# Optimization experiments

Measured on AMD Instinct MI355X. Metric: run time of the kernel, lower is better.

## Reference

```python
import jax, jax.numpy as jnp
import numpy as np

N_NODES = 100000
N_EDGES = 300000


def _nnconv(x, src, dst, edge_attr, w, b, root, bias, in_dim, out_dim):
    # PyG NNConv with aggr='add': W_e = nn(edge_attr_e).reshape(in, out)
    # msg_e = x[src_e] @ W_e ; out_i = sum_e->i msg_e + x_i @ root + bias
    W = (edge_attr @ w.T + b).reshape(-1, in_dim, out_dim)        # [E, in, out]
    msg = jnp.einsum('ei,eio->eo', x[src], W)                     # [E, out]
    agg = jax.ops.segment_sum(msg, dst, num_segments=x.shape[0])  # [N, out]
    return agg + x @ root + bias


def setup_inputs() -> dict:
    key = jax.random.key(0)
    ks = jax.random.split(key, 16)
    x = jax.random.normal(ks[0], (N_NODES, 2), dtype=jnp.float32)
    edge_index = jax.random.randint(ks[1], (2, N_EDGES), 0, N_NODES)
    edge_attr = jax.random.uniform(ks[2], (N_EDGES, 2), dtype=jnp.float32)

    def lin(k, out_d, in_d):
        s = 1.0 / np.sqrt(in_d)
        kw, kb = jax.random.split(k)
        w = jax.random.uniform(kw, (out_d, in_d), minval=-s, maxval=s)
        b = jax.random.uniform(kb, (out_d,), minval=-s, maxval=s)
        return w, b

    nn1_w, nn1_b = lin(ks[3], 64, 2)      # edge MLP for conv1: 2 -> 2*32
    nn2_w, nn2_b = lin(ks[4], 1024, 2)    # edge MLP for conv2: 2 -> 32*32
    root1 = jax.random.normal(ks[5], (2, 32)) * (1.0 / np.sqrt(2))
    bias1 = jnp.zeros((32,), dtype=jnp.float32)
    root2 = jax.random.normal(ks[6], (32, 32)) * (1.0 / np.sqrt(32))
    bias2 = jnp.zeros((32,), dtype=jnp.float32)
    fc1_w, fc1_b = lin(ks[7], 32, 32)
    fc2_w, fc2_b = lin(ks[8], 1, 32)
    return {
        'x': x, 'edge_index': edge_index, 'edge_attr': edge_attr,
        'nn1_w': nn1_w, 'nn1_b': nn1_b, 'root1': root1, 'bias1': bias1,
        'nn2_w': nn2_w, 'nn2_b': nn2_b, 'root2': root2, 'bias2': bias2,
        'fc1_w': fc1_w, 'fc1_b': fc1_b, 'fc2_w': fc2_w, 'fc2_b': fc2_b,
    }


def reference(x, edge_index, edge_attr, nn1_w, nn1_b, root1, bias1,
              nn2_w, nn2_b, root2, bias2, fc1_w, fc1_b, fc2_w, fc2_b):
    src, dst = edge_index[0], edge_index[1]
    h = jax.nn.relu(_nnconv(x, src, dst, edge_attr, nn1_w, nn1_b, root1, bias1, 2, 32))
    h = jax.nn.relu(_nnconv(h, src, dst, edge_attr, nn2_w, nn2_b, root2, bias2, 32, 32))
    h = jax.nn.relu(h @ fc1_w.T + fc1_b)
    return h @ fc2_w.T + fc2_b  # [N, 1]
```

## Files before the change

### kernel.cpp

```cpp
#include <hip/hip_runtime.h>

#define N_NODES 100000
#define N_EDGES 300000
#define CAP 32
#define NPAIRS (N_NODES / 2)
#define NT 64
#define NTILES ((N_NODES + NT - 1) / NT)
#define PAD 129

__global__ __launch_bounds__(256) void zero_cnt_kernel(int4* __restrict__ p,
                                                       int n4)
{
    int i = blockIdx.x * 256 + threadIdx.x;
    if (i < n4) p[i] = make_int4(0, 0, 0, 0);
}

__global__ __launch_bounds__(256) void scatter_kernel(
    const int* __restrict__ src, const int* __restrict__ dst,
    const float* __restrict__ ea,
    int* __restrict__ cnt, float4* __restrict__ slots)
{
    int e = blockIdx.x * 256 + threadIdx.x;
    if (e >= N_EDGES) return;
    int s = src[e], d = dst[e];
    float2 a = ((const float2*)ea)[e];
    int pos = atomicAdd(&cnt[d], 1);
    if (pos < CAP)
        slots[(size_t)d * CAP + pos] = make_float4(__int_as_float(s), a.x, a.y, 0.f);
}

__global__ __launch_bounds__(256) void prepack_kernel(
    const float* __restrict__ nn2_w, const float* __restrict__ nn2_b,
    const float* __restrict__ root2, const float* __restrict__ fc1_w,
    float* __restrict__ Wt, float* __restrict__ Ft)
{
    int t = blockIdx.x * 256 + threadIdx.x;
    if (t < 4096) {
        int i = t >> 5, o = t & 31;
        int ii = i & 31;
        float v;
        if (i < 32)      v = nn2_w[(ii * 32 + o) * 2];
        else if (i < 64) v = nn2_w[(ii * 32 + o) * 2 + 1];
        else if (i < 96) v = nn2_b[ii * 32 + o];
        else             v = root2[ii * 32 + o];
        Wt[i * 32 + o] = v;
    }
    if (t < 1024) {
        int o = t >> 5, j = t & 31;
        Ft[o * 32 + j] = fc1_w[j * 32 + o];
    }
}

__global__ __launch_bounds__(256) void layer1a_kernel(
    const float* __restrict__ x, const int* __restrict__ cnt,
    const float4* __restrict__ slots,
    const float* __restrict__ nn1_w, const float* __restrict__ nn1_b,
    const float* __restrict__ root1, const float* __restrict__ bias1,
    float* __restrict__ h1)
{
    int t = threadIdx.x;
    int wv = t >> 6, lane = t & 63, o = lane & 31, hihalf = lane >> 5;
    int pair = blockIdx.x * 4 + wv;
    if (pair >= NPAIRS) return;
    int n = pair * 2 + hihalf;
    int c = min(cnt[n], CAP);
    float u0 = 0.f, u1 = 0.f, u2 = 0.f, u3 = 0.f, u4 = 0.f, u5 = 0.f;
    if (o < c) {
        float4 sl = slots[(size_t)n * CAP + o];
        int s = __float_as_int(sl.x);
        float2 xv = ((const float2*)x)[s];
        u0 = xv.x * sl.y; u1 = xv.x * sl.z;
        u2 = xv.y * sl.y; u3 = xv.y * sl.z;
        u4 = xv.x;        u5 = xv.y;
    }
    #pragma unroll
    for (int m = 1; m < 32; m <<= 1) {
        u0 += __shfl_xor(u0, m, 32);
        u1 += __shfl_xor(u1, m, 32);
        u2 += __shfl_xor(u2, m, 32);
        u3 += __shfl_xor(u3, m, 32);
        u4 += __shfl_xor(u4, m, 32);
        u5 += __shfl_xor(u5, m, 32);
    }
    float2 w0 = ((const float2*)nn1_w)[o];
    float2 w1 = ((const float2*)nn1_w)[32 + o];
    float2 xn = ((const float2*)x)[n];
    float agg = u0 * w0.x + u1 * w0.y + u2 * w1.x + u3 * w1.y
              + u4 * nn1_b[o] + u5 * nn1_b[32 + o];
    float h = agg + fmaf(xn.x, root1[o], fmaf(xn.y, root1[32 + o], bias1[o]));
    h1[(size_t)n * 32 + o] = fmaxf(h, 0.f);
}

__global__ __launch_bounds__(512) void fused2_kernel(
    const float* __restrict__ h1, const int* __restrict__ cnt,
    const float4* __restrict__ slots,
    const float* __restrict__ Wt, const float* __restrict__ Ft,
    const float* __restrict__ bias2,
    const float* __restrict__ fc1_b, const float* __restrict__ fc2_w,
    const float* __restrict__ fc2_b, float* __restrict__ out)
{
    __shared__ float ld[NT][PAD];
    __shared__ float h2s[NT][33];
    float* psf = &ld[0][0];

    int t = threadIdx.x;
    int hw = t >> 5;
    int o  = t & 31;
    int wv = t >> 6;
    int wvu = __builtin_amdgcn_readfirstlane(wv);
    int lane = t & 63;
    int tb = blockIdx.x * NT;

    int na = tb + hw, nb = tb + 16 + hw, nc = tb + 32 + hw, nd = tb + 48 + hw;
    int ca = (na < N_NODES) ? cnt[na] : 0;
    int cb2 = (nb < N_NODES) ? cnt[nb] : 0;
    int cc = (nc < N_NODES) ? cnt[nc] : 0;
    int cd = (nd < N_NODES) ? cnt[nd] : 0;
    #pragma unroll
    for (int r = 0; r < 4; ++r) {
        int ln = r * 16 + hw;
        int n = tb + ln;
        int c = (r == 0) ? ca : (r == 1) ? cb2 : (r == 2) ? cc : cd;
        c = min(c, CAP);
        if (n < N_NODES) {
            float U = 0.f, V = 0.f, Wc = 0.f;
            for (int j0 = 0; j0 < c; j0 += 4) {
                bool g1 = j0 + 1 < c, g2 = j0 + 2 < c, g3 = j0 + 3 < c;
                float4 s0 = slots[(size_t)n * CAP + j0];
                float4 s1 = g1 ? slots[(size_t)n * CAP + j0 + 1] : s0;
                float4 s2 = g2 ? slots[(size_t)n * CAP + j0 + 2] : s0;
                float4 s3 = g3 ? slots[(size_t)n * CAP + j0 + 3] : s0;
                int i0 = __float_as_int(s0.x), i1 = __float_as_int(s1.x);
                int i2 = __float_as_int(s2.x), i3 = __float_as_int(s3.x);
                float v0 = h1[(size_t)i0 * 32 + o];
                float v1 = h1[(size_t)i1 * 32 + o];
                float v2 = h1[(size_t)i2 * 32 + o];
                float v3 = h1[(size_t)i3 * 32 + o];
                U = fmaf(s0.y, v0, U);
                U = fmaf(g1 ? s1.y : 0.f, v1, U);
                U = fmaf(g2 ? s2.y : 0.f, v2, U);
                U = fmaf(g3 ? s3.y : 0.f, v3, U);
                V = fmaf(s0.z, v0, V);
                V = fmaf(g1 ? s1.z : 0.f, v1, V);
                V = fmaf(g2 ? s2.z : 0.f, v2, V);
                V = fmaf(g3 ? s3.z : 0.f, v3, V);
                Wc += v0;
                Wc = fmaf(g1 ? 1.f : 0.f, v1, Wc);
                Wc = fmaf(g2 ? 1.f : 0.f, v2, Wc);
                Wc = fmaf(g3 ? 1.f : 0.f, v3, Wc);
            }
            float T = h1[(size_t)n * 32 + o];
            ld[ln][o]      = U;
            ld[ln][32 + o] = V;
            ld[ln][64 + o] = Wc;
            ld[ln][96 + o] = T;
        }
    }
    __syncthreads();

    {
        int cb = 4 * wvu;
        float4 bb = *(const float4*)(bias2 + cb);
        float a0 = bb.x, a1 = bb.y, a2 = bb.z, a3 = bb.w;
        for (int i = 0; i < 128; ++i) {
            float hv = ld[lane][i];
            float4 wA = *(const float4*)(Wt + i * 32 + cb);
            a0 = fmaf(hv, wA.x, a0); a1 = fmaf(hv, wA.y, a1);
            a2 = fmaf(hv, wA.z, a2); a3 = fmaf(hv, wA.w, a3);
        }
        h2s[lane][cb + 0] = fmaxf(a0, 0.f);
        h2s[lane][cb + 1] = fmaxf(a1, 0.f);
        h2s[lane][cb + 2] = fmaxf(a2, 0.f);
        h2s[lane][cb + 3] = fmaxf(a3, 0.f);
    }
    __syncthreads();

    {
        int cb = 4 * wvu;
        float4 fb = *(const float4*)(fc1_b + cb);
        float z0 = fb.x, z1 = fb.y, z2 = fb.z, z3 = fb.w;
        for (int i = 0; i < 32; ++i) {
            float hv = h2s[lane][i];
            float4 fA = *(const float4*)(Ft + i * 32 + cb);
            z0 = fmaf(hv, fA.x, z0); z1 = fmaf(hv, fA.y, z1);
            z2 = fmaf(hv, fA.z, z2); z3 = fmaf(hv, fA.w, z3);
        }
        float4 cw = *(const float4*)(fc2_w + cb);
        float po = fmaxf(z0, 0.f) * cw.x + fmaxf(z1, 0.f) * cw.y
                 + fmaxf(z2, 0.f) * cw.z + fmaxf(z3, 0.f) * cw.w;
        psf[wv * NT + lane] = po;
    }
    __syncthreads();
    if (wv == 0) {
        int n = tb + lane;
        if (n < N_NODES) {
            float s = psf[lane]            + psf[NT + lane]
                    + psf[2 * NT + lane]   + psf[3 * NT + lane]
                    + psf[4 * NT + lane]   + psf[5 * NT + lane]
                    + psf[6 * NT + lane]   + psf[7 * NT + lane];
            out[n] = s + fc2_b[0];
        }
    }
}

extern "C" void kernel_launch(void* const* d_in, const int* in_sizes, int n_in,
                              void* d_out, int out_size, void* d_ws, size_t ws_size,
                              hipStream_t stream) {
    const float* x      = (const float*)d_in[0];
    const int*   ei     = (const int*)d_in[1];
    const float* ea     = (const float*)d_in[2];
    const float* nn1_w  = (const float*)d_in[3];
    const float* nn1_b  = (const float*)d_in[4];
    const float* root1  = (const float*)d_in[5];
    const float* bias1  = (const float*)d_in[6];
    const float* nn2_w  = (const float*)d_in[7];
    const float* nn2_b  = (const float*)d_in[8];
    const float* root2  = (const float*)d_in[9];
    const float* bias2  = (const float*)d_in[10];
    const float* fc1_w  = (const float*)d_in[11];
    const float* fc1_b  = (const float*)d_in[12];
    const float* fc2_w  = (const float*)d_in[13];
    const float* fc2_b  = (const float*)d_in[14];
    float* out = (float*)d_out;

    float* ws = (float*)d_ws;
    int*    cnt   = (int*)ws;
    float4* slots = (float4*)(ws + 262144);
    float*  h1    = ws + 262144 + (size_t)N_NODES * CAP * 4;
    float*  Wt    = h1 + (size_t)N_NODES * 32;
    float*  Ft    = Wt + 4096;

    const int* src = ei;
    const int* dst = ei + N_EDGES;

    zero_cnt_kernel<<<(N_NODES / 4 + 255) / 256, 256, 0, stream>>>(
        (int4*)cnt, N_NODES / 4);
    prepack_kernel<<<16, 256, 0, stream>>>(
        nn2_w, nn2_b, root2, fc1_w, Wt, Ft);
    scatter_kernel<<<(N_EDGES + 255) / 256, 256, 0, stream>>>(
        src, dst, ea, cnt, slots);
    layer1a_kernel<<<(NPAIRS + 3) / 4, 256, 0, stream>>>(
        x, cnt, slots, nn1_w, nn1_b, root1, bias1, h1);
    fused2_kernel<<<NTILES, 512, 0, stream>>>(
        h1, cnt, slots, Wt, Ft, bias2, fc1_b, fc2_w, fc2_b, out);
}
```

Measured before the change: 96.06 us.

## Split fused layer-2 kernel into separate gather and matvec/FC kernels

Splits the fused second-layer kernel into a gather kernel that writes per-node U/V/W aggregates to a global buffer and a dense matvec/FC kernel that loads them coalesced into shared memory. The intent is to give the irregular gather higher occupancy, free of the large LDS footprint and block-wide syncs, and to make the dense stage regular. The cost is an extra global round trip of about 96 floats per node and an extra launch. Inner loops are also unrolled, and the last tile reads past the valid nodes into adjacent workspace.

```diff
diff --git a/kernel.cpp b/kernel.cpp
--- a/kernel.cpp
+++ b/kernel.cpp
@@ -91,9 +91,48 @@
     h1[(size_t)n * 32 + o] = fmaxf(h, 0.f);
 }
 
-__global__ __launch_bounds__(512) void fused2_kernel(
+__global__ __launch_bounds__(256) void gather_uvw_kernel(
     const float* __restrict__ h1, const int* __restrict__ cnt,
-    const float4* __restrict__ slots,
+    const float4* __restrict__ slots, float* __restrict__ UVW)
+{
+    int t = threadIdx.x, o = t & 31;
+    int n = blockIdx.x * 8 + (t >> 5);
+    if (n >= N_NODES) return;
+    int c = min(cnt[n], CAP);
+    float U = 0.f, V = 0.f, W = 0.f;
+    for (int j0 = 0; j0 < c; j0 += 4) {
+        bool g1 = j0 + 1 < c, g2 = j0 + 2 < c, g3 = j0 + 3 < c;
+        float4 s0 = slots[(size_t)n * CAP + j0];
+        float4 s1 = g1 ? slots[(size_t)n * CAP + j0 + 1] : s0;
+        float4 s2 = g2 ? slots[(size_t)n * CAP + j0 + 2] : s0;
+        float4 s3 = g3 ? slots[(size_t)n * CAP + j0 + 3] : s0;
+        int i0 = __float_as_int(s0.x), i1 = __float_as_int(s1.x);
+        int i2 = __float_as_int(s2.x), i3 = __float_as_int(s3.x);
+        float v0 = h1[(size_t)i0 * 32 + o];
+        float v1 = h1[(size_t)i1 * 32 + o];
+        float v2 = h1[(size_t)i2 * 32 + o];
+        float v3 = h1[(size_t)i3 * 32 + o];
+        U = fmaf(s0.y, v0, U);
+        U = fmaf(g1 ? s1.y : 0.f, v1, U);
+        U = fmaf(g2 ? s2.y : 0.f, v2, U);
+        U = fmaf(g3 ? s3.y : 0.f, v3, U);
+        V = fmaf(s0.z, v0, V);
+        V = fmaf(g1 ? s1.z : 0.f, v1, V);
+        V = fmaf(g2 ? s2.z : 0.f, v2, V);
+        V = fmaf(g3 ? s3.z : 0.f, v3, V);
+        W += v0;
+        W = fmaf(g1 ? 1.f : 0.f, v1, W);
+        W = fmaf(g2 ? 1.f : 0.f, v2, W);
+        W = fmaf(g3 ? 1.f : 0.f, v3, W);
+    }
+    size_t b = (size_t)n * 96;
+    UVW[b + o]      = U;
+    UVW[b + 32 + o] = V;
+    UVW[b + 64 + o] = W;
+}
+
+__global__ __launch_bounds__(512, 6) void matvec_fc_kernel(
+    const float* __restrict__ UVW, const float* __restrict__ h1,
     const float* __restrict__ Wt, const float* __restrict__ Ft,
     const float* __restrict__ bias2,
     const float* __restrict__ fc1_b, const float* __restrict__ fc2_w,
@@ -104,57 +143,30 @@
     float* psf = &ld[0][0];
 
     int t = threadIdx.x;
-    int hw = t >> 5;
-    int o  = t & 31;
     int wv = t >> 6;
     int wvu = __builtin_amdgcn_readfirstlane(wv);
     int lane = t & 63;
     int tb = blockIdx.x * NT;
 
-    int na = tb + hw, nb = tb + 16 + hw, nc = tb + 32 + hw, nd = tb + 48 + hw;
-    int ca = (na < N_NODES) ? cnt[na] : 0;
-    int cb2 = (nb < N_NODES) ? cnt[nb] : 0;
-    int cc = (nc < N_NODES) ? cnt[nc] : 0;
-    int cd = (nd < N_NODES) ? cnt[nd] : 0;
-    #pragma unroll
-    for (int r = 0; r < 4; ++r) {
-        int ln = r * 16 + hw;
-        int n = tb + ln;
-        int c = (r == 0) ? ca : (r == 1) ? cb2 : (r == 2) ? cc : cd;
-        c = min(c, CAP);
-        if (n < N_NODES) {
-            float U = 0.f, V = 0.f, Wc = 0.f;
-            for (int j0 = 0; j0 < c; j0 += 4) {
-                bool g1 = j0 + 1 < c, g2 = j0 + 2 < c, g3 = j0 + 3 < c;
-                float4 s0 = slots[(size_t)n * CAP + j0];
-                float4 s1 = g1 ? slots[(size_t)n * CAP + j0 + 1] : s0;
-                float4 s2 = g2 ? slots[(size_t)n * CAP + j0 + 2] : s0;
-                float4 s3 = g3 ? slots[(size_t)n * CAP + j0 + 3] : s0;
-                int i0 = __float_as_int(s0.x), i1 = __float_as_int(s1.x);
-                int i2 = __float_as_int(s2.x), i3 = __float_as_int(s3.x);
-                float v0 = h1[(size_t)i0 * 32 + o];
-                float v1 = h1[(size_t)i1 * 32 + o];
-                float v2 = h1[(size_t)i2 * 32 + o];
-                float v3 = h1[(size_t)i3 * 32 + o];
-                U = fmaf(s0.y, v0, U);
-                U = fmaf(g1 ? s1.y : 0.f, v1, U);
-                U = fmaf(g2 ? s2.y : 0.f, v2, U);
-                U = fmaf(g3 ? s3.y : 0.f, v3, U);
-                V = fmaf(s0.z, v0, V);
-                V = fmaf(g1 ? s1.z : 0.f, v1, V);
-                V = fmaf(g2 ? s2.z : 0.f, v2, V);
-                V = fmaf(g3 ? s3.z : 0.f, v3, V);
-                Wc += v0;
-                Wc = fmaf(g1 ? 1.f : 0.f, v1, Wc);
-                Wc = fmaf(g2 ? 1.f : 0.f, v2, Wc);
-                Wc = fmaf(g3 ? 1.f : 0.f, v3, Wc);
-            }
-            float T = h1[(size_t)n * 32 + o];
-            ld[ln][o]      = U;
-            ld[ln][32 + o] = V;
-            ld[ln][64 + o] = Wc;
-            ld[ln][96 + o] = T;
-        }
+    {
+        const float4* uvw4 = (const float4*)(UVW + (size_t)tb * 96);
+        #pragma unroll
+        for (int it = 0; it < 3; ++it) {
+            int f4i = it * 512 + t;
+            float4 v = uvw4[f4i];
+            int node = f4i / 24, c4 = (f4i % 24) * 4;
+            ld[node][c4]     = v.x;
+            ld[node][c4 + 1] = v.y;
+            ld[node][c4 + 2] = v.z;
+            ld[node][c4 + 3] = v.w;
+        }
+        const float4* h14 = (const float4*)(h1 + (size_t)tb * 32);
+        float4 v = h14[t];
+        int node = t >> 3, c4 = 96 + (t & 7) * 4;
+        ld[node][c4]     = v.x;
+        ld[node][c4 + 1] = v.y;
+        ld[node][c4 + 2] = v.z;
+        ld[node][c4 + 3] = v.w;
     }
     __syncthreads();
 
@@ -162,6 +174,7 @@
         int cb = 4 * wvu;
         float4 bb = *(const float4*)(bias2 + cb);
         float a0 = bb.x, a1 = bb.y, a2 = bb.z, a3 = bb.w;
+        #pragma unroll 8
         for (int i = 0; i < 128; ++i) {
             float hv = ld[lane][i];
             float4 wA = *(const float4*)(Wt + i * 32 + cb);
@@ -179,6 +192,7 @@
         int cb = 4 * wvu;
         float4 fb = *(const float4*)(fc1_b + cb);
         float z0 = fb.x, z1 = fb.y, z2 = fb.z, z3 = fb.w;
+        #pragma unroll 8
         for (int i = 0; i < 32; ++i) {
             float hv = h2s[lane][i];
             float4 fA = *(const float4*)(Ft + i * 32 + cb);
@@ -188,16 +202,17 @@
         float4 cw = *(const float4*)(fc2_w + cb);
         float po = fmaxf(z0, 0.f) * cw.x + fmaxf(z1, 0.f) * cw.y
                  + fmaxf(z2, 0.f) * cw.z + fmaxf(z3, 0.f) * cw.w;
+        __syncthreads();
         psf[wv * NT + lane] = po;
     }
     __syncthreads();
     if (wv == 0) {
         int n = tb + lane;
         if (n < N_NODES) {
-            float s = psf[lane]            + psf[NT + lane]
-                    + psf[2 * NT + lane]   + psf[3 * NT + lane]
-                    + psf[4 * NT + lane]   + psf[5 * NT + lane]
-                    + psf[6 * NT + lane]   + psf[7 * NT + lane];
+            float s = psf[lane]          + psf[NT + lane]
+                    + psf[2 * NT + lane] + psf[3 * NT + lane]
+                    + psf[4 * NT + lane] + psf[5 * NT + lane]
+                    + psf[6 * NT + lane] + psf[7 * NT + lane];
             out[n] = s + fc2_b[0];
         }
     }
@@ -227,7 +242,8 @@
     int*    cnt   = (int*)ws;
     float4* slots = (float4*)(ws + 262144);
     float*  h1    = ws + 262144 + (size_t)N_NODES * CAP * 4;
-    float*  Wt    = h1 + (size_t)N_NODES * 32;
+    float*  UVW   = h1 + (size_t)N_NODES * 32;
+    float*  Wt    = UVW + (size_t)N_NODES * 96;
     float*  Ft    = Wt + 4096;
 
     const int* src = ei;
@@ -241,6 +257,8 @@
         src, dst, ea, cnt, slots);
     layer1a_kernel<<<(NPAIRS + 3) / 4, 256, 0, stream>>>(
         x, cnt, slots, nn1_w, nn1_b, root1, bias1, h1);
-    fused2_kernel<<<NTILES, 512, 0, stream>>>(
-        h1, cnt, slots, Wt, Ft, bias2, fc1_b, fc2_w, fc2_b, out);
-}
+    gather_uvw_kernel<<<(N_NODES + 7) / 8, 256, 0, stream>>>(
+        h1, cnt, slots, UVW);
+    matvec_fc_kernel<<<NTILES, 512, 0, stream>>>(
+        UVW, h1, Wt, Ft, bias2, fc1_b, fc2_w, fc2_b, out);
+}
```

Measured after the change: 94.61 us. About the same (-1.5%).
